# Kernel optimization log

Measured on AMD Instinct MI355X. Metric: run time of the kernel, lower is better.

The kernel has to match this reference:

```python
import jax, jax.numpy as jnp
import numpy as np

H = 128   # hidden_size
E = 100   # embedding/input_size
V = 1000  # vocabulary_size
FD = 512  # feature_extractor_dim
N, TQ, TA = 512, 64, 64


def _cell(x, h, c, Wih, Whh, b):
    # PyTorch LSTM cell, gate order i,f,g,o; b = b_ih + b_hh fused.
    z = x @ Wih.T + h @ Whh.T + b
    i, f, g, o = jnp.split(z, 4, axis=-1)
    c = jax.nn.sigmoid(f) * c + jax.nn.sigmoid(i) * jnp.tanh(g)
    h = jax.nn.sigmoid(o) * jnp.tanh(c)
    return h, c


def setup_inputs() -> dict:
    key = jax.random.key(0)
    ks = iter(jax.random.split(key, 40))
    def w(shape, s=0.08):
        return (s * jax.random.normal(next(ks), shape)).astype(jnp.float32)
    inp = {
        "questions": jax.random.randint(next(ks), (N, TQ), 0, V),
        "answers": jax.random.randint(next(ks), (N, TA), 0, V),
        "answer_lens": jax.random.randint(next(ks), (N,), 1, TA + 1),
        "img": w((FD,), 1.0),  # pre-extracted image features (feature_extractor = identity)
        "emb": w((V, E), 0.1),
    }
    for p in ("enc", "dec"):
        inp[p + "_Wih0"] = w((4 * H, E)); inp[p + "_Whh0"] = w((4 * H, H)); inp[p + "_b0"] = w((4 * H,))
        inp[p + "_Wih1"] = w((4 * H, H)); inp[p + "_Whh1"] = w((4 * H, H)); inp[p + "_b1"] = w((4 * H,))
    inp["Wk"] = w((H, H)); inp["bk"] = w((H,))
    inp["Wout"] = w((V, 3 * H + FD)); inp["bout"] = w((V,))
    return inp


def reference(questions, answers, answer_lens, img, emb,
              enc_Wih0, enc_Whh0, enc_b0, enc_Wih1, enc_Whh1, enc_b1,
              dec_Wih0, dec_Whh0, dec_b0, dec_Wih1, dec_Whh1, dec_b1,
              Wk, bk, Wout, bout):
    n, tq = questions.shape
    # ---- encode: 2-layer LSTM over all questions (batched), keys projection ----
    qe = emb[questions]                               # [N,TQ,E]
    z = jnp.zeros((n, H), emb.dtype)
    def enc_step(carry, x_t):
        h0, c0, h1, c1 = carry
        h0, c0 = _cell(x_t, h0, c0, enc_Wih0, enc_Whh0, enc_b0)
        h1, c1 = _cell(h0, h1, c1, enc_Wih1, enc_Whh1, enc_b1)
        return (h0, c0, h1, c1), h1
    (eh0, ec0, eh1, ec1), outs = jax.lax.scan(enc_step, (z, z, z, z), qe.swapaxes(0, 1))
    keys = outs.swapaxes(0, 1) @ Wk.T + bk            # [N,TQ,H]; decode uses keys as values too

    # ---- decode: sequential over questions (history carry), scan over timesteps ----
    ae = emb[answers]                                  # [N,TA,E]
    mask = (jnp.arange(answers.shape[1])[None, :] < answer_lens[:, None]).astype(emb.dtype)

    def q_step(history, xs):
        emb_q, k_q, h0, c0, h1, c1, m_q = xs
        def t_step(carry, x_t):
            h0, c0, h1, c1 = carry
            h0, c0 = _cell(x_t, h0, c0, dec_Wih0, dec_Whh0, dec_b0)
            h1, c1 = _cell(h0, h1, c1, dec_Wih1, dec_Whh1, dec_b1)
            ctx = jax.nn.softmax(k_q @ h1) @ k_q       # dot-product attention, v := k (as in source)
            feat = jnp.concatenate([h1, ctx, history, img], axis=-1)  # [3H+FD]
            return (h0, c0, h1, c1), feat @ Wout.T + bout
        carry, logits = jax.lax.scan(t_step, (h0, c0, h1, c1), emb_q)
        return carry[2], logits * m_q[:, None]         # history <- last-layer h; mask ragged tail

    _, logits = jax.lax.scan(q_step, jnp.zeros((H,), emb.dtype),
                             (ae, keys, eh0, ec0, eh1, ec1, mask))
    return logits                                      # [N,TA,V], zero-padded past answer_lens
```

## Files before the change

### kernel.cpp

```cpp
#include <hip/hip_runtime.h>
#include <stdint.h>

#define HD   128
#define ED   100
#define VD   1000
#define FDV  512
#define NS   512
#define TT   64
#define MT   (NS*TT)

typedef __attribute__((ext_vector_type(8))) short  short8;
typedef __attribute__((ext_vector_type(4))) float  f32x4;

typedef const __attribute__((address_space(1))) uint16_t* gas_u16;
typedef __attribute__((address_space(3))) uint16_t*       las_u16;

__device__ __forceinline__ float blo(uint32_t u){ return __uint_as_float(u << 16); }
__device__ __forceinline__ float bhi(uint32_t u){ return __uint_as_float(u & 0xffff0000u); }
__device__ __forceinline__ uint16_t f2bf(float f){
  uint32_t x = __float_as_uint(f);
  return (uint16_t)((x + 0x7fffu + ((x >> 16) & 1u)) >> 16);
}
__device__ __forceinline__ float sigf(float x){ return 1.f/(1.f+__expf(-x)); }
__device__ __forceinline__ float ftanh(float x){
  float ax = fabsf(x);
  float e = __expf(-2.f*ax);
  float t = (1.f - e) / (1.f + e);
  return copysignf(t, x);
}

struct ConvJob { const float* s; uint16_t* d; int R, R0, C, Cp; };
struct ConvJobs { ConvJob j[12]; };

__global__ void k_convert(ConvJobs jobs){
  int stride = gridDim.x * blockDim.x;
  int tid0 = blockIdx.x * blockDim.x + threadIdx.x;
  for (int ji = 0; ji < 12; ++ji){
    const ConvJob jb = jobs.j[ji];
    int total = jb.R * jb.Cp;
    for (int i = tid0; i < total; i += stride){
      int r = i / jb.Cp, c = i - r*jb.Cp;
      float v = (r < jb.R0 && c < jb.C) ? jb.s[(size_t)r*jb.C + c] : 0.f;
      jb.d[i] = f2bf(v);
    }
  }
}

__global__ void k_gather(const uint16_t* __restrict__ embP, const int* __restrict__ tok,
                         uint16_t* __restrict__ out){
  int i = blockIdx.x * blockDim.x + threadIdx.x;
  if (i >= MT*16) return;
  int m = i >> 4, c8 = i & 15;
  int v = tok[m];
  ((uint4*)(out + (size_t)m*128))[c8] = ((const uint4*)(embP + (size_t)v*128))[c8];
}

template<int MODE>
__global__ __launch_bounds__(256) void k_gemm(
    const uint16_t* __restrict__ A, const uint16_t* __restrict__ W,
    const float* __restrict__ bias, void* __restrict__ out,
    int N, int K, const int* __restrict__ lens)
{
  __shared__ __align__(16) uint16_t lsA[128][32];
  __shared__ __align__(16) uint16_t lsB[128][32];
  const int tid = threadIdx.x;
  const int n0 = blockIdx.x * 128, m0 = blockIdx.y * 128;
  const int l = tid & 63, w = tid >> 6;
  const int wm = (w >> 1) * 64, wn = (w & 1) * 64;
  const int fr = l & 15, fo = (l >> 4) * 8;
  const int srow = w*16 + (l >> 2);
  const int sce  = (l & 3) * 8;
  f32x4 acc[4][4] = {};
  for (int kt = 0; kt < K; kt += 32) {
    #pragma unroll
    for (int u = 0; u < 2; ++u) {
      const int row = u*64 + srow;
      const int lo  = w*512 + u*2048;
      __builtin_amdgcn_global_load_lds(
          (gas_u16)(A + (size_t)(m0 + row) * K + kt + sce),
          (las_u16)(&lsA[0][0] + lo), 16, 0, 0);
      __builtin_amdgcn_global_load_lds(
          (gas_u16)(W + (size_t)(n0 + row) * K + kt + sce),
          (las_u16)(&lsB[0][0] + lo), 16, 0, 0);
    }
    __syncthreads();
    short8 af[4], bfv[4];
    #pragma unroll
    for (int i = 0; i < 4; ++i) af[i]  = *(const short8*)(&lsA[wm + i*16 + fr][fo]);
    #pragma unroll
    for (int j = 0; j < 4; ++j) bfv[j] = *(const short8*)(&lsB[wn + j*16 + fr][fo]);
    #pragma unroll
    for (int i = 0; i < 4; ++i)
      #pragma unroll
      for (int j = 0; j < 4; ++j)
        acc[i][j] = __builtin_amdgcn_mfma_f32_16x16x32_bf16(af[i], bfv[j], acc[i][j], 0, 0, 0);
    __syncthreads();
  }
  const int r0 = (l >> 4) * 4, cc = l & 15;
  #pragma unroll
  for (int j = 0; j < 4; ++j) {
    int col = n0 + wn + j*16 + cc;
    if (col >= N) continue;
    float bv = bias[col];
    #pragma unroll
    for (int i = 0; i < 4; ++i) {
      #pragma unroll
      for (int r = 0; r < 4; ++r) {
        int row = m0 + wm + i*16 + r0 + r;
        float v = acc[i][j][r] + bv;
        if (MODE == 1) {
          ((uint16_t*)out)[(size_t)row * N + col] = f2bf(v);
        } else if (MODE == 2) {
          int t = row & 63, n = row >> 6;
          if (t >= lens[n]) v = 0.f;
          ((float*)out)[(size_t)row * N + col] = v;
        } else {
          ((float*)out)[(size_t)row * N + col] = v;
        }
      }
    }
  }
}

__global__ __launch_bounds__(512) void k_lstm_mfma(
    const uint16_t* __restrict__ X,
    const uint16_t* __restrict__ Whh,
    const float* __restrict__ h0i, const float* __restrict__ c0i,
    uint16_t* __restrict__ hout,
    float* __restrict__ hfin, float* __restrict__ cfin)
{
  __shared__ __align__(16) uint16_t hbuf[2][16][136];
  const int n0 = blockIdx.x * 16;
  const int w = threadIdx.x >> 6, l = threadIdx.x & 63;
  const int s = l & 15;
  const int hi4 = l >> 4;
  const int j0 = w*16 + hi4*4;

  short8 afr[4][4];
  #pragma unroll
  for (int g = 0; g < 4; ++g)
    #pragma unroll
    for (int kk = 0; kk < 4; ++kk)
      afr[g][kk] = *(const short8*)(Whh + (size_t)(g*128 + w*16 + s)*128 + kk*32 + hi4*8);

  f32x4 cst = {0.f, 0.f, 0.f, 0.f};
  if (c0i) cst = *(const f32x4*)(c0i + (size_t)(n0+s)*128 + j0);
  {
    uint16_t hb[4] = {0,0,0,0};
    if (h0i) {
      float4 hv = *(const float4*)(h0i + (size_t)(n0+s)*128 + j0);
      hb[0]=f2bf(hv.x); hb[1]=f2bf(hv.y); hb[2]=f2bf(hv.z); hb[3]=f2bf(hv.w);
    }
    *(uint2*)(&hbuf[0][s][j0]) = *(const uint2*)hb;
  }
  __syncthreads();

  const uint16_t* Xp = X + (size_t)(n0+s)*TT*512 + j0;
  uint2 xv[4], xvn[4];
  #pragma unroll
  for (int g = 0; g < 4; ++g) xv[g] = *(const uint2*)(Xp + g*128);

  float hfv[4] = {0.f,0.f,0.f,0.f};
  for (int t = 0; t < TT; ++t) {
    const int rb = t & 1;
    if (t + 1 < TT) {
      const uint16_t* Xn = Xp + (size_t)(t+1)*512;
      #pragma unroll
      for (int g = 0; g < 4; ++g) xvn[g] = *(const uint2*)(Xn + g*128);
    }
    short8 bfr[4];
    #pragma unroll
    for (int kk = 0; kk < 4; ++kk)
      bfr[kk] = *(const short8*)(&hbuf[rb][s][kk*32 + hi4*8]);
    f32x4 acc[4] = {{0.f,0.f,0.f,0.f},{0.f,0.f,0.f,0.f},{0.f,0.f,0.f,0.f},{0.f,0.f,0.f,0.f}};
    #pragma unroll
    for (int kk = 0; kk < 4; ++kk)
      #pragma unroll
      for (int g = 0; g < 4; ++g)
        acc[g] = __builtin_amdgcn_mfma_f32_16x16x32_bf16(afr[g][kk], bfr[kk], acc[g], 0, 0, 0);
    uint16_t hb[4];
    #pragma unroll
    for (int r = 0; r < 4; ++r) {
      uint32_t wi = (r & 2) ? xv[0].y : xv[0].x;
      uint32_t wf = (r & 2) ? xv[1].y : xv[1].x;
      uint32_t wg = (r & 2) ? xv[2].y : xv[2].x;
      uint32_t wo = (r & 2) ? xv[3].y : xv[3].x;
      float zi = acc[0][r] + ((r & 1) ? bhi(wi) : blo(wi));
      float zf = acc[1][r] + ((r & 1) ? bhi(wf) : blo(wf));
      float zg = acc[2][r] + ((r & 1) ? bhi(wg) : blo(wg));
      float zo = acc[3][r] + ((r & 1) ? bhi(wo) : blo(wo));
      float cn = sigf(zf) * cst[r] + sigf(zi) * ftanh(zg);
      float h  = sigf(zo) * ftanh(cn);
      cst[r] = cn;
      hfv[r] = h;
      hb[r] = f2bf(h);
    }
    *(uint2*)(&hbuf[rb ^ 1][s][j0]) = *(const uint2*)hb;
    *(uint2*)(hout + ((size_t)(n0+s)*TT + t)*HD + j0) = *(const uint2*)hb;
    if (t + 1 < TT) {
      #pragma unroll
      for (int g = 0; g < 4; ++g) xv[g] = xvn[g];
    }
    __syncthreads();
  }
  if (hfin) *(float4*)(hfin + (size_t)(n0+s)*128 + j0) = make_float4(hfv[0],hfv[1],hfv[2],hfv[3]);
  if (cfin) *(float4*)(cfin + (size_t)(n0+s)*128 + j0) = make_float4(cst[0],cst[1],cst[2],cst[3]);
}

__global__ __launch_bounds__(256) void k_attn(
    const float* __restrict__ keys,
    const uint16_t* __restrict__ h1,
    const uint16_t* __restrict__ imgb,
    uint16_t* __restrict__ feat)
{
  __shared__ float ks[64][129];
  __shared__ float ps[4][64];
  const int n = blockIdx.x;
  for (int i = threadIdx.x; i < 64*128; i += 256)
    ks[i >> 7][i & 127] = keys[(size_t)n*8192 + i];
  const int w = threadIdx.x >> 6, l = threadIdx.x & 63;
  uint32_t hd = 0;
  if (n > 0) hd = ((const uint32_t*)(h1 + ((size_t)(n-1)*64 + 63)*128))[l];
  const uint4 iv = ((const uint4*)imgb)[l];
  __syncthreads();
  for (int tt = 0; tt < 16; ++tt) {
    const int t = tt*4 + w;
    const size_t m = (size_t)n*64 + t;
    const uint4* hp = (const uint4*)(h1 + m*128);
    float s = 0.f;
    #pragma unroll
    for (int k = 0; k < 16; ++k) {
      uint4 hv = hp[k];
      s += ks[l][8*k+0]*blo(hv.x) + ks[l][8*k+1]*bhi(hv.x)
         + ks[l][8*k+2]*blo(hv.y) + ks[l][8*k+3]*bhi(hv.y)
         + ks[l][8*k+4]*blo(hv.z) + ks[l][8*k+5]*bhi(hv.z)
         + ks[l][8*k+6]*blo(hv.w) + ks[l][8*k+7]*bhi(hv.w);
    }
    float mx = s;
    #pragma unroll
    for (int o = 32; o; o >>= 1) mx = fmaxf(mx, __shfl_xor(mx, o));
    float p = __expf(s - mx);
    float sm = p;
    #pragma unroll
    for (int o = 32; o; o >>= 1) sm += __shfl_xor(sm, o);
    p /= sm;
    ps[w][l] = p;
    float c0 = 0.f, c1 = 0.f;
    #pragma unroll
    for (int q = 0; q < 64; ++q) {
      float pq = ps[w][q];
      c0 += pq * ks[q][l];
      c1 += pq * ks[q][l + 64];
    }
    uint16_t* fr_ = feat + m*896;
    ((uint32_t*)fr_)[l] = ((const uint32_t*)(h1 + m*128))[l];
    fr_[128 + l] = f2bf(c0);
    fr_[192 + l] = f2bf(c1);
    ((uint32_t*)(fr_ + 256))[l] = hd;
    ((uint4*)(fr_ + 384))[l] = iv;
  }
}

extern "C" void kernel_launch(void* const* d_in, const int* in_sizes, int n_in,
                              void* d_out, int out_size, void* d_ws, size_t ws_size,
                              hipStream_t stream) {
  const int*   questions = (const int*)d_in[0];
  const int*   answers   = (const int*)d_in[1];
  const int*   lens      = (const int*)d_in[2];
  const float* img       = (const float*)d_in[3];
  const float* emb       = (const float*)d_in[4];
  const float* eWih0 = (const float*)d_in[5],  *eWhh0 = (const float*)d_in[6],  *eB0 = (const float*)d_in[7];
  const float* eWih1 = (const float*)d_in[8],  *eWhh1 = (const float*)d_in[9],  *eB1 = (const float*)d_in[10];
  const float* dWih0 = (const float*)d_in[11], *dWhh0 = (const float*)d_in[12], *dB0 = (const float*)d_in[13];
  const float* dWih1 = (const float*)d_in[14], *dWhh1 = (const float*)d_in[15], *dB1 = (const float*)d_in[16];
  const float* Wk   = (const float*)d_in[17], *bk   = (const float*)d_in[18];
  const float* Wout = (const float*)d_in[19], *bout = (const float*)d_in[20];

  char* ws = (char*)d_ws;
  size_t off = 0;
  auto alloc = [&](size_t n)->char* {
    char* p = ws + off; off += (n + 255) & ~(size_t)255; return p;
  };
  uint16_t* embP  = (uint16_t*)alloc((size_t)VD*128*2);
  uint16_t* wih0e = (uint16_t*)alloc(512*128*2);
  uint16_t* whh0e = (uint16_t*)alloc(512*128*2);
  uint16_t* wih1e = (uint16_t*)alloc(512*128*2);
  uint16_t* whh1e = (uint16_t*)alloc(512*128*2);
  uint16_t* wih0d = (uint16_t*)alloc(512*128*2);
  uint16_t* whh0d = (uint16_t*)alloc(512*128*2);
  uint16_t* wih1d = (uint16_t*)alloc(512*128*2);
  uint16_t* whh1d = (uint16_t*)alloc(512*128*2);
  uint16_t* wkb   = (uint16_t*)alloc(128*128*2);
  uint16_t* woutb = (uint16_t*)alloc((size_t)1024*896*2);
  uint16_t* imgb  = (uint16_t*)alloc(512*2);
  uint16_t* embBuf= (uint16_t*)alloc((size_t)MT*128*2);
  uint16_t* Xbuf  = (uint16_t*)alloc((size_t)MT*512*2);
  uint16_t* hA    = (uint16_t*)alloc((size_t)MT*128*2);
  uint16_t* h1b   = (uint16_t*)alloc((size_t)MT*128*2);
  float*    keysf = (float*)   alloc((size_t)MT*128*4);
  uint16_t* feat  = (uint16_t*)alloc((size_t)MT*896*2);
  float* eh0 = (float*)alloc(NS*128*4);
  float* ec0 = (float*)alloc(NS*128*4);
  float* eh1 = (float*)alloc(NS*128*4);
  float* ec1 = (float*)alloc(NS*128*4);
  if (off > ws_size) return;

  ConvJobs jobs;
  jobs.j[0]  = {emb,   embP,  VD,  VD,  ED,  128};
  jobs.j[1]  = {eWih0, wih0e, 512, 512, ED,  128};
  jobs.j[2]  = {eWhh0, whh0e, 512, 512, 128, 128};
  jobs.j[3]  = {eWih1, wih1e, 512, 512, 128, 128};
  jobs.j[4]  = {eWhh1, whh1e, 512, 512, 128, 128};
  jobs.j[5]  = {dWih0, wih0d, 512, 512, ED,  128};
  jobs.j[6]  = {dWhh0, whh0d, 512, 512, 128, 128};
  jobs.j[7]  = {dWih1, wih1d, 512, 512, 128, 128};
  jobs.j[8]  = {dWhh1, whh1d, 512, 512, 128, 128};
  jobs.j[9]  = {Wk,    wkb,   128, 128, 128, 128};
  jobs.j[10] = {Wout,  woutb, 1024, VD, 896, 896};
  jobs.j[11] = {img,   imgb,  1,   1,   512, 512};
  hipLaunchKernelGGL(k_convert, dim3(1024), dim3(256), 0, stream, jobs);

  hipLaunchKernelGGL(k_gather, dim3(MT*16/256), dim3(256), 0, stream, embP, questions, embBuf);
  hipLaunchKernelGGL(k_gemm<1>, dim3(4, MT/128), dim3(256), 0, stream, embBuf, wih0e, eB0, Xbuf, 512, 128, nullptr);
  hipLaunchKernelGGL(k_lstm_mfma, dim3(NS/16), dim3(512), 0, stream, Xbuf, whh0e, (const float*)nullptr, (const float*)nullptr, hA, eh0, ec0);
  hipLaunchKernelGGL(k_gemm<1>, dim3(4, MT/128), dim3(256), 0, stream, hA, wih1e, eB1, Xbuf, 512, 128, nullptr);
  hipLaunchKernelGGL(k_lstm_mfma, dim3(NS/16), dim3(512), 0, stream, Xbuf, whh1e, (const float*)nullptr, (const float*)nullptr, h1b, eh1, ec1);
  hipLaunchKernelGGL(k_gemm<0>, dim3(1, MT/128), dim3(256), 0, stream, h1b, wkb, bk, keysf, 128, 128, nullptr);

  hipLaunchKernelGGL(k_gather, dim3(MT*16/256), dim3(256), 0, stream, embP, answers, embBuf);
  hipLaunchKernelGGL(k_gemm<1>, dim3(4, MT/128), dim3(256), 0, stream, embBuf, wih0d, dB0, Xbuf, 512, 128, nullptr);
  hipLaunchKernelGGL(k_lstm_mfma, dim3(NS/16), dim3(512), 0, stream, Xbuf, whh0d, eh0, ec0, hA, (float*)nullptr, (float*)nullptr);
  hipLaunchKernelGGL(k_gemm<1>, dim3(4, MT/128), dim3(256), 0, stream, hA, wih1d, dB1, Xbuf, 512, 128, nullptr);
  hipLaunchKernelGGL(k_lstm_mfma, dim3(NS/16), dim3(512), 0, stream, Xbuf, whh1d, eh1, ec1, h1b, (float*)nullptr, (float*)nullptr);

  hipLaunchKernelGGL(k_attn, dim3(NS), dim3(256), 0, stream, keysf, h1b, imgb, feat);
  hipLaunchKernelGGL(k_gemm<2>, dim3(8, MT/128), dim3(256), 0, stream, feat, woutb, bout, d_out, VD, 896, lens);
}
```

Baseline: 901.5 us.

## Fuse embedding gather into input GEMM, reorder gate layout, lighten LSTM barrier

The separate embedding-gather kernel is removed. The input-projection GEMM now loads embedding rows directly through token indices, which saves a launch and a round trip of the gathered buffer through memory. The GEMM epilogue writes the gate pre-activations in a time-major, 16-sequence-tiled layout, so each LSTM block's per-timestep reads are contiguous across its 16 sequences. The LSTM's per-step __syncthreads is replaced with an LDS-only waitcnt plus s_barrier, so each step no longer waits on outstanding global loads.

Result: no change. 890.7 us (-1.2%).

```diff
diff --git a/kernel.cpp b/kernel.cpp
--- a/kernel.cpp
+++ b/kernel.cpp
@@ -27,6 +27,10 @@
   float e = __expf(-2.f*ax);
   float t = (1.f - e) / (1.f + e);
   return copysignf(t, x);
+}
+__device__ __forceinline__ void lds_barrier(){
+  asm volatile("s_waitcnt lgkmcnt(0)" ::: "memory");
+  __builtin_amdgcn_s_barrier();
 }
 
 struct ConvJob { const float* s; uint16_t* d; int R, R0, C, Cp; };
@@ -46,20 +50,11 @@
   }
 }
 
-__global__ void k_gather(const uint16_t* __restrict__ embP, const int* __restrict__ tok,
-                         uint16_t* __restrict__ out){
-  int i = blockIdx.x * blockDim.x + threadIdx.x;
-  if (i >= MT*16) return;
-  int m = i >> 4, c8 = i & 15;
-  int v = tok[m];
-  ((uint4*)(out + (size_t)m*128))[c8] = ((const uint4*)(embP + (size_t)v*128))[c8];
-}
-
 template<int MODE>
 __global__ __launch_bounds__(256) void k_gemm(
     const uint16_t* __restrict__ A, const uint16_t* __restrict__ W,
     const float* __restrict__ bias, void* __restrict__ out,
-    int N, int K, const int* __restrict__ lens)
+    int N, int K, const int* __restrict__ lens, const int* __restrict__ tok)
 {
   __shared__ __align__(16) uint16_t lsA[128][32];
   __shared__ __align__(16) uint16_t lsB[128][32];
@@ -70,18 +65,24 @@
   const int fr = l & 15, fo = (l >> 4) * 8;
   const int srow = w*16 + (l >> 2);
   const int sce  = (l & 3) * 8;
+  const int ar0 = m0 + srow, ar1 = m0 + 64 + srow;
+  const size_t ab0 = (tok ? (size_t)tok[ar0] : (size_t)ar0) * K;
+  const size_t ab1 = (tok ? (size_t)tok[ar1] : (size_t)ar1) * K;
   f32x4 acc[4][4] = {};
   for (int kt = 0; kt < K; kt += 32) {
-    #pragma unroll
-    for (int u = 0; u < 2; ++u) {
-      const int row = u*64 + srow;
-      const int lo  = w*512 + u*2048;
+    {
       __builtin_amdgcn_global_load_lds(
-          (gas_u16)(A + (size_t)(m0 + row) * K + kt + sce),
-          (las_u16)(&lsA[0][0] + lo), 16, 0, 0);
+          (gas_u16)(A + ab0 + kt + sce),
+          (las_u16)(&lsA[0][0] + w*512), 16, 0, 0);
       __builtin_amdgcn_global_load_lds(
-          (gas_u16)(W + (size_t)(n0 + row) * K + kt + sce),
-          (las_u16)(&lsB[0][0] + lo), 16, 0, 0);
+          (gas_u16)(W + (size_t)(n0 + srow) * K + kt + sce),
+          (las_u16)(&lsB[0][0] + w*512), 16, 0, 0);
+      __builtin_amdgcn_global_load_lds(
+          (gas_u16)(A + ab1 + kt + sce),
+          (las_u16)(&lsA[0][0] + w*512 + 2048), 16, 0, 0);
+      __builtin_amdgcn_global_load_lds(
+          (gas_u16)(W + (size_t)(n0 + 64 + srow) * K + kt + sce),
+          (las_u16)(&lsB[0][0] + w*512 + 2048), 16, 0, 0);
     }
     __syncthreads();
     short8 af[4], bfv[4];
@@ -108,8 +109,10 @@
       for (int r = 0; r < 4; ++r) {
         int row = m0 + wm + i*16 + r0 + r;
         float v = acc[i][j][r] + bv;
-        if (MODE == 1) {
-          ((uint16_t*)out)[(size_t)row * N + col] = f2bf(v);
+        if (MODE == 3) {
+          int t = row & 63, n = row >> 6;
+          size_t prow = ((size_t)(n >> 4)*64 + (size_t)t)*16 + (n & 15);
+          ((uint16_t*)out)[prow * 512 + col] = f2bf(v);
         } else if (MODE == 2) {
           int t = row & 63, n = row >> 6;
           if (t >= lens[n]) v = 0.f;
@@ -155,7 +158,7 @@
   }
   __syncthreads();
 
-  const uint16_t* Xp = X + (size_t)(n0+s)*TT*512 + j0;
+  const uint16_t* Xp = X + (size_t)blockIdx.x * TT * 8192 + s*512 + j0;
   uint2 xv[4], xvn[4];
   #pragma unroll
   for (int g = 0; g < 4; ++g) xv[g] = *(const uint2*)(Xp + g*128);
@@ -164,7 +167,7 @@
   for (int t = 0; t < TT; ++t) {
     const int rb = t & 1;
     if (t + 1 < TT) {
-      const uint16_t* Xn = Xp + (size_t)(t+1)*512;
+      const uint16_t* Xn = Xp + (size_t)(t+1)*8192;
       #pragma unroll
       for (int g = 0; g < 4; ++g) xvn[g] = *(const uint2*)(Xn + g*128);
     }
@@ -201,7 +204,7 @@
       #pragma unroll
       for (int g = 0; g < 4; ++g) xv[g] = xvn[g];
     }
-    __syncthreads();
+    lds_barrier();
   }
   if (hfin) *(float4*)(hfin + (size_t)(n0+s)*128 + j0) = make_float4(hfv[0],hfv[1],hfv[2],hfv[3]);
   if (cfin) *(float4*)(cfin + (size_t)(n0+s)*128 + j0) = make_float4(cst[0],cst[1],cst[2],cst[3]);
@@ -293,7 +296,6 @@
   uint16_t* wkb   = (uint16_t*)alloc(128*128*2);
   uint16_t* woutb = (uint16_t*)alloc((size_t)1024*896*2);
   uint16_t* imgb  = (uint16_t*)alloc(512*2);
-  uint16_t* embBuf= (uint16_t*)alloc((size_t)MT*128*2);
   uint16_t* Xbuf  = (uint16_t*)alloc((size_t)MT*512*2);
   uint16_t* hA    = (uint16_t*)alloc((size_t)MT*128*2);
   uint16_t* h1b   = (uint16_t*)alloc((size_t)MT*128*2);
@@ -320,19 +322,17 @@
   jobs.j[11] = {img,   imgb,  1,   1,   512, 512};
   hipLaunchKernelGGL(k_convert, dim3(1024), dim3(256), 0, stream, jobs);
 
-  hipLaunchKernelGGL(k_gather, dim3(MT*16/256), dim3(256), 0, stream, embP, questions, embBuf);
-  hipLaunchKernelGGL(k_gemm<1>, dim3(4, MT/128), dim3(256), 0, stream, embBuf, wih0e, eB0, Xbuf, 512, 128, nullptr);
+  hipLaunchKernelGGL(k_gemm<3>, dim3(4, MT/128), dim3(256), 0, stream, embP, wih0e, eB0, Xbuf, 512, 128, nullptr, questions);
   hipLaunchKernelGGL(k_lstm_mfma, dim3(NS/16), dim3(512), 0, stream, Xbuf, whh0e, (const float*)nullptr, (const float*)nullptr, hA, eh0, ec0);
-  hipLaunchKernelGGL(k_gemm<1>, dim3(4, MT/128), dim3(256), 0, stream, hA, wih1e, eB1, Xbuf, 512, 128, nullptr);
+  hipLaunchKernelGGL(k_gemm<3>, dim3(4, MT/128), dim3(256), 0, stream, hA, wih1e, eB1, Xbuf, 512, 128, nullptr, nullptr);
   hipLaunchKernelGGL(k_lstm_mfma, dim3(NS/16), dim3(512), 0, stream, Xbuf, whh1e, (const float*)nullptr, (const float*)nullptr, h1b, eh1, ec1);
-  hipLaunchKernelGGL(k_gemm<0>, dim3(1, MT/128), dim3(256), 0, stream, h1b, wkb, bk, keysf, 128, 128, nullptr);
-
-  hipLaunchKernelGGL(k_gather, dim3(MT*16/256), dim3(256), 0, stream, embP, answers, embBuf);
-  hipLaunchKernelGGL(k_gemm<1>, dim3(4, MT/128), dim3(256), 0, stream, embBuf, wih0d, dB0, Xbuf, 512, 128, nullptr);
+  hipLaunchKernelGGL(k_gemm<0>, dim3(1, MT/128), dim3(256), 0, stream, h1b, wkb, bk, keysf, 128, 128, nullptr, nullptr);
+
+  hipLaunchKernelGGL(k_gemm<3>, dim3(4, MT/128), dim3(256), 0, stream, embP, wih0d, dB0, Xbuf, 512, 128, nullptr, answers);
   hipLaunchKernelGGL(k_lstm_mfma, dim3(NS/16), dim3(512), 0, stream, Xbuf, whh0d, eh0, ec0, hA, (float*)nullptr, (float*)nullptr);
-  hipLaunchKernelGGL(k_gemm<1>, dim3(4, MT/128), dim3(256), 0, stream, hA, wih1d, dB1, Xbuf, 512, 128, nullptr);
+  hipLaunchKernelGGL(k_gemm<3>, dim3(4, MT/128), dim3(256), 0, stream, hA, wih1d, dB1, Xbuf, 512, 128, nullptr, nullptr);
   hipLaunchKernelGGL(k_lstm_mfma, dim3(NS/16), dim3(512), 0, stream, Xbuf, whh1d, eh1, ec1, h1b, (float*)nullptr, (float*)nullptr);
 
   hipLaunchKernelGGL(k_attn, dim3(NS), dim3(256), 0, stream, keysf, h1b, imgb, feat);
-  hipLaunchKernelGGL(k_gemm<2>, dim3(8, MT/128), dim3(256), 0, stream, feat, woutb, bout, d_out, VD, 896, lens);
-}
+  hipLaunchKernelGGL(k_gemm<2>, dim3(8, MT/128), dim3(256), 0, stream, feat, woutb, bout, d_out, VD, 896, lens, nullptr);
+}
```
